# Kernel tuning notes

Hardware: AMD Instinct MI355X
Metric: run time of the kernel (lower is better)

Reference implementation:

```python
import jax, jax.numpy as jnp
import numpy as np

D_MODEL = 512
N_HEADS = 8
D_K = D_MODEL // N_HEADS


def setup_inputs() -> dict:
    key = jax.random.key(0)
    ks = jax.random.split(key, 7)
    s = 1.0 / np.sqrt(D_MODEL)
    return {
        "x": jax.random.normal(ks[0], (2, 4096, D_MODEL), dtype=jnp.float32),
        "W_q": jax.random.normal(ks[1], (D_MODEL, D_MODEL), dtype=jnp.float32) * s,
        "W_k": jax.random.normal(ks[2], (D_MODEL, D_MODEL), dtype=jnp.float32) * s,
        "W_v": jax.random.normal(ks[3], (D_MODEL, D_MODEL), dtype=jnp.float32) * s,
        "b_v": jax.random.normal(ks[4], (D_MODEL,), dtype=jnp.float32) * s,
        "W_o": jax.random.normal(ks[5], (D_MODEL, D_MODEL), dtype=jnp.float32) * s,
        "b_o": jax.random.normal(ks[6], (D_MODEL,), dtype=jnp.float32) * s,
    }


def _split_heads(t):
    # [N, S, d_model] -> [N, H, S, d_k]
    N, S, _ = t.shape
    return t.reshape(N, S, N_HEADS, D_K).transpose(0, 2, 1, 3)


def reference(x, W_q, W_k, W_v, b_v, W_o, b_o):
    N, S, _ = x.shape
    # nn.Linear computes x @ W.T (+ b)
    Q = _split_heads(x @ W_q.T)
    K = _split_heads(x @ W_k.T)
    V = _split_heads(x @ W_v.T + b_v)
    scale = jnp.sqrt(jnp.asarray(D_K, x.dtype))
    scores = jnp.einsum('nhqd,nhkd->nhqk', Q, K) / scale  # [N,H,S,S]
    causal = jnp.tril(jnp.ones((S, S), dtype=bool))
    scores = jnp.where(causal, scores, -jnp.inf)
    attn = jax.nn.softmax(scores, axis=-1)
    out = jnp.einsum('nhqk,nhkd->nhqd', attn, V)  # [N,H,S,d_k]
    out = out.transpose(0, 2, 1, 3).reshape(N, S, D_MODEL)
    return out @ W_o.T + b_o
```

## Files before the change

### kernel.cpp

```cpp
#include <hip/hip_runtime.h>
#include <hip/hip_bf16.h>

#define NB 2
#define SEQ 4096
#define DM 512
#define NH 8
#define DKH 64
#define MTOT (NB*SEQ)

typedef __attribute__((ext_vector_type(4))) float f32x4;
typedef __attribute__((ext_vector_type(16))) float f32x16;
typedef __attribute__((ext_vector_type(8))) short bf16x8;
typedef __attribute__((ext_vector_type(2))) unsigned uint2v;

__device__ inline unsigned short f2bf(float f) {
    union { float f; unsigned int u; } v; v.f = f;
    unsigned int r = v.u + 0x7FFFu + ((v.u >> 16) & 1u);
    return (unsigned short)(r >> 16);
}

#define QSCALE 0.18033688011112042f

__global__ void cast_kernel(const float* __restrict__ x, const float* __restrict__ wq,
                            const float* __restrict__ wk, const float* __restrict__ wv,
                            const float* __restrict__ wo, unsigned short* __restrict__ dst) {
    const int NX = MTOT*DM;
    const int NW = DM*DM;
    int i4 = blockIdx.x * blockDim.x + threadIdx.x;
    long e = (long)i4 * 4;
    if (e >= NX + 4L*NW) return;
    const float* src; long off;
    if (e < NX)           { src = x;  off = e; }
    else if (e < NX+NW)   { src = wq; off = e - NX; }
    else if (e < NX+2*NW) { src = wk; off = e - NX - NW; }
    else if (e < NX+3*NW) { src = wv; off = e - NX - 2*NW; }
    else                  { src = wo; off = e - NX - 3*NW; }
    float4 v = *reinterpret_cast<const float4*>(src + off);
    ushort4 o;
    o.x = f2bf(v.x); o.y = f2bf(v.y); o.z = f2bf(v.z); o.w = f2bf(v.w);
    *reinterpret_cast<ushort4*>(dst + e) = o;
}

template<int MODE>
__global__ __launch_bounds__(256, 2) void gemm_bt(
    const unsigned short* __restrict__ A,
    const unsigned short* __restrict__ B,
    const float* __restrict__ bias,
    unsigned short* __restrict__ Qh, unsigned short* __restrict__ Kh,
    unsigned short* __restrict__ Vt,
    float* __restrict__ Cout)
{
    const int K = 512;
    __shared__ __align__(16) unsigned short As[128*64];
    __shared__ __align__(16) unsigned short Bs[128*64];
    int tid = threadIdx.x;
    int wid = tid >> 6, lane = tid & 63;
    int wr = wid >> 1, wc = wid & 1;
    int brow = blockIdx.x * 128;
    int bcol = blockIdx.y * 128;
    int l15 = lane & 15, l4 = lane >> 4;

    f32x4 acc[4][4] = {};

    for (int kt = 0; kt < K/64; ++kt) {
        __syncthreads();
        #pragma unroll
        for (int i = 0; i < 4; ++i) {
            int rbase = i*32 + wid*8;
            int row = rbase + (lane >> 3);
            int csrc = (lane & 7) ^ (row & 7);
            const unsigned short* asrc = A + (long)(brow+row)*K + kt*64 + csrc*8;
            __builtin_amdgcn_global_load_lds(
                (const __attribute__((address_space(1))) unsigned int*)asrc,
                (__attribute__((address_space(3))) unsigned int*)&As[rbase*64], 16, 0, 0);
            const unsigned short* bsrc = B + (long)(bcol+row)*K + kt*64 + csrc*8;
            __builtin_amdgcn_global_load_lds(
                (const __attribute__((address_space(1))) unsigned int*)bsrc,
                (__attribute__((address_space(3))) unsigned int*)&Bs[rbase*64], 16, 0, 0);
        }
        __syncthreads();
        #pragma unroll
        for (int kk = 0; kk < 2; ++kk) {
            bf16x8 af[4], bfr[4];
            #pragma unroll
            for (int mi = 0; mi < 4; ++mi) {
                int row = wr*64 + mi*16 + l15;
                int colb = (kk*32 + l4*8) * 2;
                af[mi] = *reinterpret_cast<const bf16x8*>(
                    reinterpret_cast<const char*>(As) + row*128 + (colb ^ ((row&7)<<4)));
            }
            #pragma unroll
            for (int ni = 0; ni < 4; ++ni) {
                int row = wc*64 + ni*16 + l15;
                int colb = (kk*32 + l4*8) * 2;
                bfr[ni] = *reinterpret_cast<const bf16x8*>(
                    reinterpret_cast<const char*>(Bs) + row*128 + (colb ^ ((row&7)<<4)));
            }
            #pragma unroll
            for (int mi = 0; mi < 4; ++mi)
                #pragma unroll
                for (int ni = 0; ni < 4; ++ni)
                    acc[mi][ni] = __builtin_amdgcn_mfma_f32_16x16x32_bf16(af[mi], bfr[ni], acc[mi][ni], 0, 0, 0);
        }
    }

    #pragma unroll
    for (int mi = 0; mi < 4; ++mi) {
        #pragma unroll
        for (int ni = 0; ni < 4; ++ni) {
            #pragma unroll
            for (int r = 0; r < 4; ++r) {
                int row = brow + wr*64 + mi*16 + l4*4 + r;
                int col = bcol + wc*64 + ni*16 + l15;
                float v = acc[mi][ni][r];
                if (MODE == 0) {
                    int which = col >> 9;
                    int cw = col & 511;
                    int h = cw >> 6, d = cw & 63;
                    int b = row >> 12, s = row & 4095;
                    int bh = b*NH + h;
                    if (which == 0) {
                        Qh[((long)(bh*SEQ + s))*DKH + d] = f2bf(v * QSCALE);
                    } else if (which == 1) {
                        Kh[((long)(bh*SEQ + s))*DKH + d] = f2bf(v);
                    } else {
                        Vt[((long)(bh*DKH + d))*SEQ + s] = f2bf(v + bias[cw]);
                    }
                } else {
                    Cout[(long)row*DM + col] = v + bias[col];
                }
            }
        }
    }
}

__global__ __launch_bounds__(256, 2) void attn_kernel(
    const unsigned short* __restrict__ Qh,
    const unsigned short* __restrict__ Kh,
    const unsigned short* __restrict__ Vt,
    unsigned short* __restrict__ Obf)
{
    __shared__ __align__(16) unsigned short Klds[2][128*64];
    __shared__ __align__(16) unsigned short Vlds[2][2*64*64];
    const int tid = threadIdx.x;
    const int wid = tid >> 6, lane = tid & 63;
    const int l31 = lane & 31;
    const int hi  = lane >> 5;
    const int bh  = blockIdx.x;
    const int ty  = blockIdx.y;
    const int tile = ty < 16 ? 31 - ty : ty - 16;

    const unsigned short* Qbase = Qh + (long)bh*SEQ*DKH;
    const unsigned short* Kbase = Kh + (long)bh*SEQ*DKH;
    const unsigned short* Vbase = Vt + (long)bh*DKH*SEQ;

    const int q0w = tile*128 + wid*32;
    const int q   = q0w + l31;
    const int nt  = tile + 1;
    const int swz = (l31 & 7) << 4;

    bf16x8 qf[4];
    #pragma unroll
    for (int kk = 0; kk < 4; ++kk)
        qf[kk] = *reinterpret_cast<const bf16x8*>(Qbase + (long)q*DKH + kk*16 + hi*8);

    auto STAGE = [&](int b, int key0) {
        #pragma unroll
        for (int ii = 0; ii < 4; ++ii) {
            const int rbase = wid*32 + ii*8;
            const int row = rbase + (lane >> 3);
            const int ck = (lane & 7) ^ (row & 7);
            const unsigned short* ksrc = Kbase + (long)(key0 + row)*DKH + ck*8;
            __builtin_amdgcn_global_load_lds(
                (const __attribute__((address_space(1))) unsigned int*)ksrc,
                (__attribute__((address_space(3))) unsigned int*)&Klds[b][rbase*64], 16, 0, 0);
        }
        #pragma unroll
        for (int jj = 0; jj < 2; ++jj) {
            #pragma unroll
            for (int ii = 0; ii < 2; ++ii) {
                const int rbase = wid*16 + ii*8;
                const int row = rbase + (lane >> 3);
                const int ck = (lane & 7) ^ (row & 7);
                const unsigned short* vsrc = Vbase + (long)row*SEQ + key0 + jj*64 + ck*8;
                __builtin_amdgcn_global_load_lds(
                    (const __attribute__((address_space(1))) unsigned int*)vsrc,
                    (__attribute__((address_space(3))) unsigned int*)&Vlds[b][jj*4096 + rbase*64], 16, 0, 0);
            }
        }
    };

    float m = -1e30f, lsum = 0.f;
    f32x16 od0 = {}, od1 = {};

    STAGE(0, 0);
    __syncthreads();
    int cur = 0;

    for (int kb = 0; kb < nt; ++kb) {
        if (kb + 1 < nt) STAGE(cur ^ 1, (kb + 1) << 7);
        const char* kl = reinterpret_cast<const char*>(Klds[cur]);
        const char* vl = reinterpret_cast<const char*>(Vlds[cur]);
        const int key0 = kb << 7;

        f32x16 s0 = {}, s1 = {}, s2 = {}, s3 = {};
        __builtin_amdgcn_s_setprio(1);
        #pragma unroll
        for (int kk = 0; kk < 4; ++kk) {
            const int co = (kk*32 + hi*16) ^ swz;
            bf16x8 kf0 = *reinterpret_cast<const bf16x8*>(kl + l31*128       + co);
            s0 = __builtin_amdgcn_mfma_f32_32x32x16_bf16(kf0, qf[kk], s0, 0, 0, 0);
            bf16x8 kf1 = *reinterpret_cast<const bf16x8*>(kl + (32+l31)*128  + co);
            s1 = __builtin_amdgcn_mfma_f32_32x32x16_bf16(kf1, qf[kk], s1, 0, 0, 0);
            bf16x8 kf2 = *reinterpret_cast<const bf16x8*>(kl + (64+l31)*128  + co);
            s2 = __builtin_amdgcn_mfma_f32_32x32x16_bf16(kf2, qf[kk], s2, 0, 0, 0);
            bf16x8 kf3 = *reinterpret_cast<const bf16x8*>(kl + (96+l31)*128  + co);
            s3 = __builtin_amdgcn_mfma_f32_32x32x16_bf16(kf3, qf[kk], s3, 0, 0, 0);
        }
        __builtin_amdgcn_s_setprio(0);

        if (key0 + 127 > q0w) {
            #pragma unroll
            for (int r = 0; r < 16; ++r) {
                const int ko = (r&3) + 8*(r>>2) + 4*hi;
                if (key0 + ko > q)      s0[r] = -1e30f;
                if (key0 + 32 + ko > q) s1[r] = -1e30f;
                if (key0 + 64 + ko > q) s2[r] = -1e30f;
                if (key0 + 96 + ko > q) s3[r] = -1e30f;
            }
        }

        float pmax = s0[0];
        #pragma unroll
        for (int r = 1; r < 16; ++r) pmax = fmaxf(pmax, s0[r]);
        #pragma unroll
        for (int r = 0; r < 16; ++r) pmax = fmaxf(pmax, fmaxf(s1[r], fmaxf(s2[r], s3[r])));
        {
            uint2v pr = __builtin_amdgcn_permlane32_swap(__float_as_uint(pmax), __float_as_uint(pmax), false, false);
            pmax = fmaxf(__uint_as_float(pr[0]), __uint_as_float(pr[1]));
        }

        if (__any(pmax > m + 6.0f)) {
            const float mn = fmaxf(m, pmax);
            const float alpha = __builtin_amdgcn_exp2f(m - mn);
            m = mn;
            lsum *= alpha;
            #pragma unroll
            for (int r = 0; r < 16; ++r) { od0[r] *= alpha; od1[r] *= alpha; }
        }

        float rs = 0.f;
        #pragma unroll
        for (int r = 0; r < 16; ++r) {
            s0[r] = __builtin_amdgcn_exp2f(s0[r] - m);
            s1[r] = __builtin_amdgcn_exp2f(s1[r] - m);
            s2[r] = __builtin_amdgcn_exp2f(s2[r] - m);
            s3[r] = __builtin_amdgcn_exp2f(s3[r] - m);
            rs += (s0[r] + s1[r]) + (s2[r] + s3[r]);
        }
        lsum += rs;

        __builtin_amdgcn_s_setprio(1);
#define PV_STEP(SV, VLS, KS, B0) do {                                              \
        unsigned c0, c1, c2, c3;                                                   \
        float t0 = SV[B0+0], t1 = SV[B0+1], t2 = SV[B0+2], t3 = SV[B0+3];          \
        float t4 = SV[B0+4], t5 = SV[B0+5], t6 = SV[B0+6], t7 = SV[B0+7];          \
        asm("v_cvt_pk_bf16_f32 %0, %1, %2" : "=v"(c0) : "v"(t0), "v"(t1));         \
        asm("v_cvt_pk_bf16_f32 %0, %1, %2" : "=v"(c1) : "v"(t2), "v"(t3));         \
        asm("v_cvt_pk_bf16_f32 %0, %1, %2" : "=v"(c2) : "v"(t4), "v"(t5));         \
        asm("v_cvt_pk_bf16_f32 %0, %1, %2" : "=v"(c3) : "v"(t6), "v"(t7));         \
        uint2v sw0 = __builtin_amdgcn_permlane32_swap(c0, c2, false, false);       \
        uint2v sw1 = __builtin_amdgcn_permlane32_swap(c1, c3, false, false);       \
        union { unsigned u[4]; bf16x8 v; } pu;                                     \
        pu.u[0] = sw0[0]; pu.u[1] = sw1[0]; pu.u[2] = sw0[1]; pu.u[3] = sw1[1];    \
        bf16x8 vf0 = *reinterpret_cast<const bf16x8*>(VLS + l31*128      + (((KS)*32 + hi*16) ^ swz)); \
        od0 = __builtin_amdgcn_mfma_f32_32x32x16_bf16(vf0, pu.v, od0, 0, 0, 0);    \
        bf16x8 vf1 = *reinterpret_cast<const bf16x8*>(VLS + (32+l31)*128 + (((KS)*32 + hi*16) ^ swz)); \
        od1 = __builtin_amdgcn_mfma_f32_32x32x16_bf16(vf1, pu.v, od1, 0, 0, 0);    \
    } while (0)
        const char* vl0 = vl;
        const char* vl1 = vl + 8192;
        PV_STEP(s0, vl0, 0, 0);
        PV_STEP(s0, vl0, 1, 8);
        PV_STEP(s1, vl0, 2, 0);
        PV_STEP(s1, vl0, 3, 8);
        PV_STEP(s2, vl1, 0, 0);
        PV_STEP(s2, vl1, 1, 8);
        PV_STEP(s3, vl1, 2, 0);
        PV_STEP(s3, vl1, 3, 8);
#undef PV_STEP
        __builtin_amdgcn_s_setprio(0);

        __syncthreads();
        cur ^= 1;
    }

    {
        uint2v pr = __builtin_amdgcn_permlane32_swap(__float_as_uint(lsum), __float_as_uint(lsum), false, false);
        lsum = __uint_as_float(pr[0]) + __uint_as_float(pr[1]);
    }
    const float rls = 1.0f / lsum;
    const long obase = (long)((bh >> 3)*SEQ + q)*DM + (bh & 7)*DKH;
    #pragma unroll
    for (int rr = 0; rr < 4; ++rr) {
        ushort4 w0, w1;
        w0.x = f2bf(od0[rr*4+0]*rls); w0.y = f2bf(od0[rr*4+1]*rls);
        w0.z = f2bf(od0[rr*4+2]*rls); w0.w = f2bf(od0[rr*4+3]*rls);
        *reinterpret_cast<ushort4*>(Obf + obase + rr*8 + hi*4) = w0;
        w1.x = f2bf(od1[rr*4+0]*rls); w1.y = f2bf(od1[rr*4+1]*rls);
        w1.z = f2bf(od1[rr*4+2]*rls); w1.w = f2bf(od1[rr*4+3]*rls);
        *reinterpret_cast<ushort4*>(Obf + obase + 32 + rr*8 + hi*4) = w1;
    }
}

extern "C" void kernel_launch(void* const* d_in, const int* in_sizes, int n_in,
                              void* d_out, int out_size, void* d_ws, size_t ws_size,
                              hipStream_t stream) {
    const float* x  = (const float*)d_in[0];
    const float* wq = (const float*)d_in[1];
    const float* wk = (const float*)d_in[2];
    const float* wv = (const float*)d_in[3];
    const float* bv = (const float*)d_in[4];
    const float* wo = (const float*)d_in[5];
    const float* bo = (const float*)d_in[6];
    float* out = (float*)d_out;

    unsigned short* ws = (unsigned short*)d_ws;
    unsigned short* Xbf  = ws;
    unsigned short* Wqkv = Xbf  + 4194304;
    unsigned short* Wob  = Wqkv + 786432;
    unsigned short* Qh   = Wob  + 262144;
    unsigned short* Kh   = Qh   + 4194304;
    unsigned short* Vt   = Kh   + 4194304;
    unsigned short* Obf  = Vt   + 4194304;

    cast_kernel<<<5120, 256, 0, stream>>>(x, wq, wk, wv, wo, Xbf);

    dim3 g1(64, 12);
    gemm_bt<0><<<g1, 256, 0, stream>>>(Xbf, Wqkv, bv, Qh, Kh, Vt, nullptr);

    dim3 g2(16, 32);
    attn_kernel<<<g2, 256, 0, stream>>>(Qh, Kh, Vt, Obf);

    dim3 g3(64, 4);
    gemm_bt<1><<<g3, 256, 0, stream>>>(Obf, Wob, bo, nullptr, nullptr, nullptr, out);
}
```

Baseline: 119.8 us.

## Pad LDS rows for K/V tiles, preload K fragments, interleave exp with PV MFMAs

Changes the LDS layout for K and V tiles so that each 8-row group is padded by 32 bytes (528-element stride), intended to cut LDS bank conflicts on the fragment reads. It also loads all K fragments into registers before the QK MFMA chain. The exponentials are now computed per 32-key chunk just before the matching PV MFMAs, so VALU work can overlap with the matrix unit. The setprio around the PV phase is removed. The trade-offs are more register pressure from the preloaded K fragments and slightly larger shared memory use.

```diff
diff --git a/kernel.cpp b/kernel.cpp
--- a/kernel.cpp
+++ b/kernel.cpp
@@ -140,8 +140,8 @@
     const unsigned short* __restrict__ Vt,
     unsigned short* __restrict__ Obf)
 {
-    __shared__ __align__(16) unsigned short Klds[2][128*64];
-    __shared__ __align__(16) unsigned short Vlds[2][2*64*64];
+    __shared__ __align__(16) unsigned short Klds[2][8448];
+    __shared__ __align__(16) unsigned short Vlds[2][8448];
     const int tid = threadIdx.x;
     const int wid = tid >> 6, lane = tid & 63;
     const int l31 = lane & 31;
@@ -157,7 +157,8 @@
     const int q0w = tile*128 + wid*32;
     const int q   = q0w + l31;
     const int nt  = tile + 1;
-    const int swz = (l31 & 7) << 4;
+    const int swz   = (l31 & 7) << 4;
+    const int lbase = (l31 >> 3)*1056 + (l31 & 7)*128;
 
     bf16x8 qf[4];
     #pragma unroll
@@ -167,25 +168,23 @@
     auto STAGE = [&](int b, int key0) {
         #pragma unroll
         for (int ii = 0; ii < 4; ++ii) {
-            const int rbase = wid*32 + ii*8;
-            const int row = rbase + (lane >> 3);
+            const int row = wid*32 + ii*8 + (lane >> 3);
             const int ck = (lane & 7) ^ (row & 7);
             const unsigned short* ksrc = Kbase + (long)(key0 + row)*DKH + ck*8;
             __builtin_amdgcn_global_load_lds(
                 (const __attribute__((address_space(1))) unsigned int*)ksrc,
-                (__attribute__((address_space(3))) unsigned int*)&Klds[b][rbase*64], 16, 0, 0);
+                (__attribute__((address_space(3))) unsigned int*)&Klds[b][(wid*4 + ii)*528], 16, 0, 0);
         }
         #pragma unroll
         for (int jj = 0; jj < 2; ++jj) {
             #pragma unroll
             for (int ii = 0; ii < 2; ++ii) {
-                const int rbase = wid*16 + ii*8;
-                const int row = rbase + (lane >> 3);
+                const int row = wid*16 + ii*8 + (lane >> 3);
                 const int ck = (lane & 7) ^ (row & 7);
                 const unsigned short* vsrc = Vbase + (long)row*SEQ + key0 + jj*64 + ck*8;
                 __builtin_amdgcn_global_load_lds(
                     (const __attribute__((address_space(1))) unsigned int*)vsrc,
-                    (__attribute__((address_space(3))) unsigned int*)&Vlds[b][jj*4096 + rbase*64], 16, 0, 0);
+                    (__attribute__((address_space(3))) unsigned int*)&Vlds[b][(jj*8 + wid*2 + ii)*528], 16, 0, 0);
             }
         }
     };
@@ -203,19 +202,22 @@
         const char* vl = reinterpret_cast<const char*>(Vlds[cur]);
         const int key0 = kb << 7;
 
+        bf16x8 kfr[4][4];
+        #pragma unroll
+        for (int kk = 0; kk < 4; ++kk) {
+            const int co = (kk*32 + hi*16) ^ swz;
+            #pragma unroll
+            for (int c = 0; c < 4; ++c)
+                kfr[kk][c] = *reinterpret_cast<const bf16x8*>(kl + lbase + c*4224 + co);
+        }
         f32x16 s0 = {}, s1 = {}, s2 = {}, s3 = {};
         __builtin_amdgcn_s_setprio(1);
         #pragma unroll
         for (int kk = 0; kk < 4; ++kk) {
-            const int co = (kk*32 + hi*16) ^ swz;
-            bf16x8 kf0 = *reinterpret_cast<const bf16x8*>(kl + l31*128       + co);
-            s0 = __builtin_amdgcn_mfma_f32_32x32x16_bf16(kf0, qf[kk], s0, 0, 0, 0);
-            bf16x8 kf1 = *reinterpret_cast<const bf16x8*>(kl + (32+l31)*128  + co);
-            s1 = __builtin_amdgcn_mfma_f32_32x32x16_bf16(kf1, qf[kk], s1, 0, 0, 0);
-            bf16x8 kf2 = *reinterpret_cast<const bf16x8*>(kl + (64+l31)*128  + co);
-            s2 = __builtin_amdgcn_mfma_f32_32x32x16_bf16(kf2, qf[kk], s2, 0, 0, 0);
-            bf16x8 kf3 = *reinterpret_cast<const bf16x8*>(kl + (96+l31)*128  + co);
-            s3 = __builtin_amdgcn_mfma_f32_32x32x16_bf16(kf3, qf[kk], s3, 0, 0, 0);
+            s0 = __builtin_amdgcn_mfma_f32_32x32x16_bf16(kfr[kk][0], qf[kk], s0, 0, 0, 0);
+            s1 = __builtin_amdgcn_mfma_f32_32x32x16_bf16(kfr[kk][1], qf[kk], s1, 0, 0, 0);
+            s2 = __builtin_amdgcn_mfma_f32_32x32x16_bf16(kfr[kk][2], qf[kk], s2, 0, 0, 0);
+            s3 = __builtin_amdgcn_mfma_f32_32x32x16_bf16(kfr[kk][3], qf[kk], s3, 0, 0, 0);
         }
         __builtin_amdgcn_s_setprio(0);
 
@@ -249,19 +251,15 @@
             for (int r = 0; r < 16; ++r) { od0[r] *= alpha; od1[r] *= alpha; }
         }
 
-        float rs = 0.f;
-        #pragma unroll
-        for (int r = 0; r < 16; ++r) {
-            s0[r] = __builtin_amdgcn_exp2f(s0[r] - m);
-            s1[r] = __builtin_amdgcn_exp2f(s1[r] - m);
-            s2[r] = __builtin_amdgcn_exp2f(s2[r] - m);
-            s3[r] = __builtin_amdgcn_exp2f(s3[r] - m);
-            rs += (s0[r] + s1[r]) + (s2[r] + s3[r]);
-        }
-        lsum += rs;
-
-        __builtin_amdgcn_s_setprio(1);
-#define PV_STEP(SV, VLS, KS, B0) do {                                              \
+        float rsc0 = 0.f, rsc1 = 0.f, rsc2 = 0.f, rsc3 = 0.f;
+#define EXP_CHUNK(SV, RS) do {                                                     \
+        _Pragma("unroll")                                                          \
+        for (int r = 0; r < 16; ++r) {                                             \
+            SV[r] = __builtin_amdgcn_exp2f(SV[r] - m);                             \
+            RS += SV[r];                                                           \
+        } } while (0)
+
+#define PV_STEP(SV, VBASE, KS, B0) do {                                            \
         unsigned c0, c1, c2, c3;                                                   \
         float t0 = SV[B0+0], t1 = SV[B0+1], t2 = SV[B0+2], t3 = SV[B0+3];          \
         float t4 = SV[B0+4], t5 = SV[B0+5], t6 = SV[B0+6], t7 = SV[B0+7];          \
@@ -273,23 +271,29 @@
         uint2v sw1 = __builtin_amdgcn_permlane32_swap(c1, c3, false, false);       \
         union { unsigned u[4]; bf16x8 v; } pu;                                     \
         pu.u[0] = sw0[0]; pu.u[1] = sw1[0]; pu.u[2] = sw0[1]; pu.u[3] = sw1[1];    \
-        bf16x8 vf0 = *reinterpret_cast<const bf16x8*>(VLS + l31*128      + (((KS)*32 + hi*16) ^ swz)); \
+        bf16x8 vf0 = *reinterpret_cast<const bf16x8*>(VBASE + lbase +        (((KS)*32 + hi*16) ^ swz)); \
         od0 = __builtin_amdgcn_mfma_f32_32x32x16_bf16(vf0, pu.v, od0, 0, 0, 0);    \
-        bf16x8 vf1 = *reinterpret_cast<const bf16x8*>(VLS + (32+l31)*128 + (((KS)*32 + hi*16) ^ swz)); \
+        bf16x8 vf1 = *reinterpret_cast<const bf16x8*>(VBASE + lbase + 4224 + (((KS)*32 + hi*16) ^ swz)); \
         od1 = __builtin_amdgcn_mfma_f32_32x32x16_bf16(vf1, pu.v, od1, 0, 0, 0);    \
     } while (0)
+
         const char* vl0 = vl;
-        const char* vl1 = vl + 8192;
+        const char* vl1 = vl + 8448;
+        EXP_CHUNK(s0, rsc0);
         PV_STEP(s0, vl0, 0, 0);
         PV_STEP(s0, vl0, 1, 8);
+        EXP_CHUNK(s1, rsc1);
         PV_STEP(s1, vl0, 2, 0);
         PV_STEP(s1, vl0, 3, 8);
+        EXP_CHUNK(s2, rsc2);
         PV_STEP(s2, vl1, 0, 0);
         PV_STEP(s2, vl1, 1, 8);
+        EXP_CHUNK(s3, rsc3);
         PV_STEP(s3, vl1, 2, 0);
         PV_STEP(s3, vl1, 3, 8);
 #undef PV_STEP
-        __builtin_amdgcn_s_setprio(0);
+#undef EXP_CHUNK
+        lsum += (rsc0 + rsc1) + (rsc2 + rsc3);
 
         __syncthreads();
         cur ^= 1;
```

Measured after the change: 121.3 us. Within noise of the previous version (+1.2%).

## Software-pipeline QK^T one block ahead and interleave exp with PV MFMAs

Applied to the files above, without the earlier changes.

Restructures the causal flash-attention loop so the QK^T MFMAs for block kb+1 are issued before the softmax of block kb, with K staged two blocks ahead and V one block ahead in split double buffers. The exp computation is also split per 32-key chunk and interleaved with the matching PV MFMAs. The aim is to overlap the softmax VALU/transcendental work with matrix-core work and hide load latency. The cost is higher register pressure from two live score sets (128 extra floats), which may lower occupancy or cause spills, plus more complex buffer indexing.

```diff
diff --git a/kernel.cpp b/kernel.cpp
--- a/kernel.cpp
+++ b/kernel.cpp
@@ -164,7 +164,7 @@
     for (int kk = 0; kk < 4; ++kk)
         qf[kk] = *reinterpret_cast<const bf16x8*>(Qbase + (long)q*DKH + kk*16 + hi*8);
 
-    auto STAGE = [&](int b, int key0) {
+    auto STAGE_K = [&](int b, int key0) {
         #pragma unroll
         for (int ii = 0; ii < 4; ++ii) {
             const int rbase = wid*32 + ii*8;
@@ -175,6 +175,8 @@
                 (const __attribute__((address_space(1))) unsigned int*)ksrc,
                 (__attribute__((address_space(3))) unsigned int*)&Klds[b][rbase*64], 16, 0, 0);
         }
+    };
+    auto STAGE_V = [&](int b, int key0) {
         #pragma unroll
         for (int jj = 0; jj < 2; ++jj) {
             #pragma unroll
@@ -193,74 +195,40 @@
     float m = -1e30f, lsum = 0.f;
     f32x16 od0 = {}, od1 = {};
 
-    STAGE(0, 0);
+    STAGE_K(0, 0);
+    if (nt > 1) STAGE_K(1, 128);
+    STAGE_V(0, 0);
     __syncthreads();
-    int cur = 0;
-
-    for (int kb = 0; kb < nt; ++kb) {
-        if (kb + 1 < nt) STAGE(cur ^ 1, (kb + 1) << 7);
-        const char* kl = reinterpret_cast<const char*>(Klds[cur]);
-        const char* vl = reinterpret_cast<const char*>(Vlds[cur]);
-        const int key0 = kb << 7;
-
-        f32x16 s0 = {}, s1 = {}, s2 = {}, s3 = {};
+
+    f32x16 sA0 = {}, sA1 = {}, sA2 = {}, sA3 = {};
+    {
+        const char* kl = reinterpret_cast<const char*>(Klds[0]);
         __builtin_amdgcn_s_setprio(1);
         #pragma unroll
         for (int kk = 0; kk < 4; ++kk) {
             const int co = (kk*32 + hi*16) ^ swz;
             bf16x8 kf0 = *reinterpret_cast<const bf16x8*>(kl + l31*128       + co);
-            s0 = __builtin_amdgcn_mfma_f32_32x32x16_bf16(kf0, qf[kk], s0, 0, 0, 0);
+            sA0 = __builtin_amdgcn_mfma_f32_32x32x16_bf16(kf0, qf[kk], sA0, 0, 0, 0);
             bf16x8 kf1 = *reinterpret_cast<const bf16x8*>(kl + (32+l31)*128  + co);
-            s1 = __builtin_amdgcn_mfma_f32_32x32x16_bf16(kf1, qf[kk], s1, 0, 0, 0);
+            sA1 = __builtin_amdgcn_mfma_f32_32x32x16_bf16(kf1, qf[kk], sA1, 0, 0, 0);
             bf16x8 kf2 = *reinterpret_cast<const bf16x8*>(kl + (64+l31)*128  + co);
-            s2 = __builtin_amdgcn_mfma_f32_32x32x16_bf16(kf2, qf[kk], s2, 0, 0, 0);
+            sA2 = __builtin_amdgcn_mfma_f32_32x32x16_bf16(kf2, qf[kk], sA2, 0, 0, 0);
             bf16x8 kf3 = *reinterpret_cast<const bf16x8*>(kl + (96+l31)*128  + co);
-            s3 = __builtin_amdgcn_mfma_f32_32x32x16_bf16(kf3, qf[kk], s3, 0, 0, 0);
+            sA3 = __builtin_amdgcn_mfma_f32_32x32x16_bf16(kf3, qf[kk], sA3, 0, 0, 0);
         }
         __builtin_amdgcn_s_setprio(0);
-
-        if (key0 + 127 > q0w) {
-            #pragma unroll
-            for (int r = 0; r < 16; ++r) {
-                const int ko = (r&3) + 8*(r>>2) + 4*hi;
-                if (key0 + ko > q)      s0[r] = -1e30f;
-                if (key0 + 32 + ko > q) s1[r] = -1e30f;
-                if (key0 + 64 + ko > q) s2[r] = -1e30f;
-                if (key0 + 96 + ko > q) s3[r] = -1e30f;
-            }
-        }
-
-        float pmax = s0[0];
-        #pragma unroll
-        for (int r = 1; r < 16; ++r) pmax = fmaxf(pmax, s0[r]);
-        #pragma unroll
-        for (int r = 0; r < 16; ++r) pmax = fmaxf(pmax, fmaxf(s1[r], fmaxf(s2[r], s3[r])));
-        {
-            uint2v pr = __builtin_amdgcn_permlane32_swap(__float_as_uint(pmax), __float_as_uint(pmax), false, false);
-            pmax = fmaxf(__uint_as_float(pr[0]), __uint_as_float(pr[1]));
-        }
-
-        if (__any(pmax > m + 6.0f)) {
-            const float mn = fmaxf(m, pmax);
-            const float alpha = __builtin_amdgcn_exp2f(m - mn);
-            m = mn;
-            lsum *= alpha;
-            #pragma unroll
-            for (int r = 0; r < 16; ++r) { od0[r] *= alpha; od1[r] *= alpha; }
-        }
-
-        float rs = 0.f;
-        #pragma unroll
-        for (int r = 0; r < 16; ++r) {
-            s0[r] = __builtin_amdgcn_exp2f(s0[r] - m);
-            s1[r] = __builtin_amdgcn_exp2f(s1[r] - m);
-            s2[r] = __builtin_amdgcn_exp2f(s2[r] - m);
-            s3[r] = __builtin_amdgcn_exp2f(s3[r] - m);
-            rs += (s0[r] + s1[r]) + (s2[r] + s3[r]);
-        }
-        lsum += rs;
-
-        __builtin_amdgcn_s_setprio(1);
+    }
+    __syncthreads();
+
+    f32x16 sB0, sB1, sB2, sB3;
+
+#define EXP_CHUNK(SV, RS) do {                                                     \
+        _Pragma("unroll")                                                          \
+        for (int r = 0; r < 16; ++r) {                                             \
+            SV[r] = __builtin_amdgcn_exp2f(SV[r] - m);                             \
+            RS += SV[r];                                                           \
+        } } while (0)
+
 #define PV_STEP(SV, VLS, KS, B0) do {                                              \
         unsigned c0, c1, c2, c3;                                                   \
         float t0 = SV[B0+0], t1 = SV[B0+1], t2 = SV[B0+2], t3 = SV[B0+3];          \
@@ -278,22 +246,95 @@
         bf16x8 vf1 = *reinterpret_cast<const bf16x8*>(VLS + (32+l31)*128 + (((KS)*32 + hi*16) ^ swz)); \
         od1 = __builtin_amdgcn_mfma_f32_32x32x16_bf16(vf1, pu.v, od1, 0, 0, 0);    \
     } while (0)
-        const char* vl0 = vl;
-        const char* vl1 = vl + 8192;
-        PV_STEP(s0, vl0, 0, 0);
-        PV_STEP(s0, vl0, 1, 8);
-        PV_STEP(s1, vl0, 2, 0);
-        PV_STEP(s1, vl0, 3, 8);
-        PV_STEP(s2, vl1, 0, 0);
-        PV_STEP(s2, vl1, 1, 8);
-        PV_STEP(s3, vl1, 2, 0);
-        PV_STEP(s3, vl1, 3, 8);
+
+#define STEP(C0, C1, C2, C3, X0, X1, X2, X3) do {                                  \
+        const int key0 = kb << 7;                                                  \
+        const bool hasN = (kb + 1 < nt);                                           \
+        if (kb + 2 < nt) STAGE_K(kb & 1, (kb + 2) << 7);                           \
+        if (hasN)        STAGE_V((kb + 1) & 1, (kb + 1) << 7);                     \
+                    \
+        if (hasN) {                                                                \
+            const char* klN = reinterpret_cast<const char*>(Klds[(kb + 1) & 1]);   \
+            X0 = (f32x16){}; X1 = (f32x16){}; X2 = (f32x16){}; X3 = (f32x16){};    \
+            __builtin_amdgcn_s_setprio(1);                                         \
+            _Pragma("unroll")                                                      \
+            for (int kk = 0; kk < 4; ++kk) {                                       \
+                const int co = (kk*32 + hi*16) ^ swz;                              \
+                bf16x8 kf0 = *reinterpret_cast<const bf16x8*>(klN + l31*128      + co); \
+                X0 = __builtin_amdgcn_mfma_f32_32x32x16_bf16(kf0, qf[kk], X0, 0, 0, 0); \
+                bf16x8 kf1 = *reinterpret_cast<const bf16x8*>(klN + (32+l31)*128 + co); \
+                X1 = __builtin_amdgcn_mfma_f32_32x32x16_bf16(kf1, qf[kk], X1, 0, 0, 0); \
+                bf16x8 kf2 = *reinterpret_cast<const bf16x8*>(klN + (64+l31)*128 + co); \
+                X2 = __builtin_amdgcn_mfma_f32_32x32x16_bf16(kf2, qf[kk], X2, 0, 0, 0); \
+                bf16x8 kf3 = *reinterpret_cast<const bf16x8*>(klN + (96+l31)*128 + co); \
+                X3 = __builtin_amdgcn_mfma_f32_32x32x16_bf16(kf3, qf[kk], X3, 0, 0, 0); \
+            }                                                                      \
+            __builtin_amdgcn_s_setprio(0);                                         \
+        }                                                                          \
+                                 \
+        if (key0 + 127 > q0w) {                                                    \
+            _Pragma("unroll")                                                      \
+            for (int r = 0; r < 16; ++r) {                                         \
+                const int ko = (r&3) + 8*(r>>2) + 4*hi;                            \
+                if (key0 + ko > q)      C0[r] = -1e30f;                            \
+                if (key0 + 32 + ko > q) C1[r] = -1e30f;                            \
+                if (key0 + 64 + ko > q) C2[r] = -1e30f;                            \
+                if (key0 + 96 + ko > q) C3[r] = -1e30f;                            \
+            }                                                                      \
+        }                                                                          \
+                                                   \
+        float pmax = C0[0];                                                        \
+        _Pragma("unroll")                                                          \
+        for (int r = 1; r < 16; ++r) pmax = fmaxf(pmax, C0[r]);                    \
+        _Pragma("unroll")                                                          \
+        for (int r = 0; r < 16; ++r) pmax = fmaxf(pmax, fmaxf(C1[r], fmaxf(C2[r], C3[r]))); \
+        {                                                                          \
+            uint2v pr = __builtin_amdgcn_permlane32_swap(__float_as_uint(pmax), __float_as_uint(pmax), false, false); \
+            pmax = fmaxf(__uint_as_float(pr[0]), __uint_as_float(pr[1]));          \
+        }                                                                          \
+                                                              \
+        if (__any(pmax > m + 6.0f)) {                                              \
+            const float mn = fmaxf(m, pmax);                                       \
+            const float alpha = __builtin_amdgcn_exp2f(m - mn);                    \
+            m = mn;                                                                \
+            lsum *= alpha;                                                         \
+            _Pragma("unroll")                                                      \
+            for (int r = 0; r < 16; ++r) { od0[r] *= alpha; od1[r] *= alpha; }     \
+        }                                                                          \
+                                                  \
+        {                                                                          \
+            const char* vl0 = reinterpret_cast<const char*>(Vlds[kb & 1]);         \
+            const char* vl1 = vl0 + 8192;                                          \
+            float rsc0 = 0.f, rsc1 = 0.f, rsc2 = 0.f, rsc3 = 0.f;                  \
+            __builtin_amdgcn_s_setprio(1);                                         \
+            EXP_CHUNK(C0, rsc0);                                                   \
+            PV_STEP(C0, vl0, 0, 0);                                                \
+            PV_STEP(C0, vl0, 1, 8);                                                \
+            EXP_CHUNK(C1, rsc1);                                                   \
+            PV_STEP(C1, vl0, 2, 0);                                                \
+            PV_STEP(C1, vl0, 3, 8);                                                \
+            EXP_CHUNK(C2, rsc2);                                                   \
+            PV_STEP(C2, vl1, 0, 0);                                                \
+            PV_STEP(C2, vl1, 1, 8);                                                \
+            EXP_CHUNK(C3, rsc3);                                                   \
+            PV_STEP(C3, vl1, 2, 0);                                                \
+            PV_STEP(C3, vl1, 3, 8);                                                \
+            __builtin_amdgcn_s_setprio(0);                                         \
+            lsum += (rsc0 + rsc1) + (rsc2 + rsc3);                                 \
+        }                                                                          \
+        __syncthreads();                                                           \
+    } while (0)
+
+    int kb = 0;
+    for (;;) {
+        STEP(sA0, sA1, sA2, sA3, sB0, sB1, sB2, sB3);
+        if (++kb >= nt) break;
+        STEP(sB0, sB1, sB2, sB3, sA0, sA1, sA2, sA3);
+        if (++kb >= nt) break;
+    }
+#undef STEP
 #undef PV_STEP
-        __builtin_amdgcn_s_setprio(0);
-
-        __syncthreads();
-        cur ^= 1;
-    }
+#undef EXP_CHUNK
 
     {
         uint2v pr = __builtin_amdgcn_permlane32_swap(__float_as_uint(lsum), __float_as_uint(lsum), false, false);
```

After: 157.0 us. 31.1% more time.
